# Optimization experiments

Hardware: AMD Instinct MI355X
Metric: run time of the kernel (lower is better)

## Reference

```python
import jax, jax.numpy as jnp
import numpy as np
from jax.ops import segment_sum

N_NODES = 100000


def _gcn_layer(x, W, b, src, dst, n_nodes):
    # DGL GraphConv with norm='both': out = D_in^{-1/2} A D_out^{-1/2} x W + b
    # degrees clamped to min 1 (DGL behavior, handles zero-degree nodes)
    ones_e = jnp.ones(src.shape[0], dtype=x.dtype)
    deg_out = jnp.clip(segment_sum(ones_e, src, num_segments=n_nodes), 1.0)
    deg_in = jnp.clip(segment_sum(ones_e, dst, num_segments=n_nodes), 1.0)
    h = x * jax.lax.rsqrt(deg_out)[:, None]            # [N, F] source norm
    agg = segment_sum(h[src], dst, num_segments=n_nodes)  # [N, F] sum over in-edges
    agg = agg * jax.lax.rsqrt(deg_in)[:, None]          # dest norm
    return agg @ W + b


def setup_inputs() -> dict:
    key = jax.random.key(0)
    k1, k2, k3, k4, k5 = jax.random.split(key, 5)
    E = 1600000
    x = jax.random.normal(k1, (N_NODES, 128), dtype=jnp.float32)
    edge_src = jax.random.randint(k2, (E,), 0, N_NODES, dtype=jnp.int32)
    edge_dst = jax.random.randint(k3, (E,), 0, N_NODES, dtype=jnp.int32)
    W1 = jax.random.normal(k4, (128, 64), dtype=jnp.float32) * (1.0 / np.sqrt(128))
    b1 = jnp.zeros((64,), dtype=jnp.float32)
    W2 = jax.random.normal(k5, (64, 64), dtype=jnp.float32) * (1.0 / np.sqrt(64))
    b2 = jnp.zeros((64,), dtype=jnp.float32)
    return {"x": x, "edge_src": edge_src, "edge_dst": edge_dst,
            "W1": W1, "b1": b1, "W2": W2, "b2": b2}


def reference(x, edge_src, edge_dst, W1, b1, W2, b2):
    h = _gcn_layer(x, W1, b1, edge_src, edge_dst, N_NODES)
    h = jax.nn.relu(h)
    out = _gcn_layer(h, W2, b2, edge_src, edge_dst, N_NODES)
    return out
```

## Files before the change

kernel.cpp:

```cpp
#include <hip/hip_runtime.h>
#include <hip/hip_fp16.h>


static inline size_t align256(size_t x) { return (x + 255) & ~(size_t)255; }

#define BKT_SHIFT 8
#define BKT_W 256
#define MAX_NBK 400
#define CAP 5120
#define SC_BLOCKS 256
#define SC_THREADS 512

typedef _Float16 f16x8 __attribute__((ext_vector_type(8)));
typedef _Float16 f16x4 __attribute__((ext_vector_type(4)));
typedef float f32x4 __attribute__((ext_vector_type(4)));

__global__ __launch_bounds__(SC_THREADS)
void scatter_atomic_kernel(const int* __restrict__ src, const int* __restrict__ dst,
                           int* __restrict__ gcnt_d, int* __restrict__ gcnt_s,
                           int* __restrict__ ebuf, unsigned char* __restrict__ sbuf,
                           int nbk, int E, int slice_len) {
    __shared__ int hd[MAX_NBK];
    __shared__ int hs[MAX_NBK];
    __shared__ int cur_d[MAX_NBK];
    __shared__ int cur_s[MAX_NBK];
    const int b = blockIdx.x;
    const int t = threadIdx.x;
    for (int i = t; i < nbk; i += SC_THREADS) { hd[i] = 0; hs[i] = 0; }
    __syncthreads();
    const int beg = b * slice_len;
    const int end = min(beg + slice_len, E);
    for (int i = beg + t; i < end; i += SC_THREADS) {
        atomicAdd(&hd[dst[i] >> BKT_SHIFT], 1);
        atomicAdd(&hs[src[i] >> BKT_SHIFT], 1);
    }
    __syncthreads();
    for (int i = t; i < nbk; i += SC_THREADS) {
        int c = hd[i];
        cur_d[i] = i * CAP + (c ? atomicAdd(&gcnt_d[i], c) : 0);
        c = hs[i];
        cur_s[i] = i * CAP + (c ? atomicAdd(&gcnt_s[i], c) : 0);
    }
    __syncthreads();
    for (int i = beg + t; i < end; i += SC_THREADS) {
        int d = dst[i], s = src[i];
        int pd = atomicAdd(&cur_d[d >> BKT_SHIFT], 1);
        ebuf[pd] = ((d & (BKT_W - 1)) << 17) | s;
        int ps = atomicAdd(&cur_s[s >> BKT_SHIFT], 1);
        sbuf[ps] = (unsigned char)(s & (BKT_W - 1));
    }
}

__global__ __launch_bounds__(256)
void bucket_csr_kernel(const int* __restrict__ ebuf,
                       const unsigned char* __restrict__ sbuf,
                       const int* __restrict__ gcnt_d, const int* __restrict__ gcnt_s,
                       int* __restrict__ csr_src,
                       int* __restrict__ cnt_in, int* __restrict__ cnt_out,
                       int* __restrict__ row_ptr,
                       int nbk, int N, int E) {
    __shared__ int cnt[BKT_W];
    __shared__ int rp[BKT_W];
    __shared__ int cur[BKT_W];
    __shared__ int cnts[BKT_W];
    __shared__ int red[256];
    __shared__ int sh_db;
    const int k = blockIdx.x;
    const int lo = k << BKT_SHIFT;
    const int span = min(BKT_W, N - lo);
    const int t = threadIdx.x;

    int s1 = 0;
    for (int i = t; i < k; i += 256) s1 += gcnt_d[i];
    red[t] = s1;
    __syncthreads();
    for (int off = 128; off >= 1; off >>= 1) {
        if (t < off) red[t] += red[t + off];
        __syncthreads();
    }
    if (t == 0) sh_db = red[0];
    __syncthreads();
    const int db = sh_db;
    const int eb = k * CAP, ee = eb + gcnt_d[k];
    const int sb = k * CAP, se = sb + gcnt_s[k];

    cnt[t] = 0; cnts[t] = 0;
    __syncthreads();
    for (int i = eb + t; i < ee; i += 256) atomicAdd(&cnt[ebuf[i] >> 17], 1);
    for (int i = sb + t; i < se; i += 256) atomicAdd(&cnts[sbuf[i]], 1);
    __syncthreads();
    rp[t] = cnt[t];
    __syncthreads();
    for (int off = 1; off < BKT_W; off <<= 1) {
        int v = (t >= off) ? rp[t - off] : 0;
        __syncthreads();
        rp[t] += v;
        __syncthreads();
    }
    if (t < span) {
        row_ptr[lo + t] = db + rp[t] - cnt[t];
        cnt_in[lo + t]  = cnt[t];
        cnt_out[lo + t] = cnts[t];
    }
    __syncthreads();
    cur[t] = db + rp[t] - cnt[t];
    __syncthreads();
    for (int i = eb + t; i < ee; i += 256) {
        int p = ebuf[i];
        int pos = atomicAdd(&cur[p >> 17], 1);
        csr_src[pos] = p & 0x1FFFF;
    }
    if (k == 0 && t == 0) row_ptr[N] = E;
}

template <int K>
__global__ __launch_bounds__(256)
void gemm_scale_kernel(const float* __restrict__ X, const float* __restrict__ W,
                       const int* __restrict__ cnt_out,
                       __half* __restrict__ Y, int N) {
    __shared__ _Float16 Wt[2][64][K + 8];
    const int t = threadIdx.x;
    {
        const int jj = t >> 2;
        const int kb = (t & 3) * (K / 4);
#pragma unroll
        for (int c8 = 0; c8 < K / 4; c8 += 8) {
            float w[8];
#pragma unroll
            for (int m = 0; m < 8; ++m) w[m] = W[(kb + c8 + m) * 64 + jj];
            f16x8 hi8, lo8;
#pragma unroll
            for (int m = 0; m < 8; ++m) {
                const _Float16 h = (_Float16)w[m];
                hi8[m] = h;
                lo8[m] = (_Float16)(w[m] - (float)h);
            }
            *(f16x8*)&Wt[0][jj][kb + c8] = hi8;
            *(f16x8*)&Wt[1][jj][kb + c8] = lo8;
        }
    }
    __syncthreads();

    const int wid  = t >> 6;
    const int lane = t & 63;
    const int col  = lane & 15;
    const int kg   = (lane >> 4) * 8;

    const int rowA = blockIdx.x * 64 + wid * 16 + col;
    const size_t xbase = (size_t)min(rowA, N - 1) * K;

    f32x4 acc0 = {}, acc1 = {}, acc2 = {}, acc3 = {};

#pragma unroll
    for (int ks = 0; ks < K; ks += 32) {
        float4 xa = *(const float4*)&X[xbase + ks + kg];
        float4 xb = *(const float4*)&X[xbase + ks + kg + 4];
        const float xs[8] = {xa.x, xa.y, xa.z, xa.w, xb.x, xb.y, xb.z, xb.w};
        f16x8 ahi, alo;
#pragma unroll
        for (int j = 0; j < 8; ++j) {
            const _Float16 h = (_Float16)xs[j];
            ahi[j] = h;
            alo[j] = (_Float16)(xs[j] - (float)h);
        }
#pragma unroll
        for (int tile = 0; tile < 4; ++tile) {
            const f16x8 bhi = *(const f16x8*)&Wt[0][col + 16 * tile][ks + kg];
            const f16x8 blo = *(const f16x8*)&Wt[1][col + 16 * tile][ks + kg];
            f32x4* acc = (tile == 0) ? &acc0 : (tile == 1) ? &acc1
                       : (tile == 2) ? &acc2 : &acc3;
            *acc = __builtin_amdgcn_mfma_f32_16x16x32_f16(ahi, bhi, *acc, 0, 0, 0);
            *acc = __builtin_amdgcn_mfma_f32_16x16x32_f16(alo, bhi, *acc, 0, 0, 0);
            *acc = __builtin_amdgcn_mfma_f32_16x16x32_f16(ahi, blo, *acc, 0, 0, 0);
        }
    }

    const int rbase = blockIdx.x * 64 + wid * 16 + (lane >> 4) * 4;
#pragma unroll
    for (int r = 0; r < 4; ++r) {
        const int rr = rbase + r;
        if (rr < N) {
            const float sc = rsqrtf((float)max(cnt_out[rr], 1));
            __half* yp = &Y[(size_t)rr * 64 + col];
            yp[0]  = __float2half_rn(acc0[r] * sc);
            yp[16] = __float2half_rn(acc1[r] * sc);
            yp[32] = __float2half_rn(acc2[r] * sc);
            yp[48] = __float2half_rn(acc3[r] * sc);
        }
    }
}

__global__ __launch_bounds__(256)
void agg_gemm_kernel(const __half* __restrict__ Y,
                     const int* __restrict__ row_ptr,
                     const int* __restrict__ csr_src,
                     const int* __restrict__ cnt_in,
                     const int* __restrict__ cnt_out,
                     const float* __restrict__ b1,
                     const float* __restrict__ W2,
                     __half* __restrict__ Y2, int N) {
    __shared__ _Float16 Hh[16][72];
    __shared__ _Float16 Hl[16][72];
    const int t = threadIdx.x;
    const int wid  = t >> 6;
    const int lane = t & 63;
    const int col  = lane & 15;
    const int kg   = (lane >> 4) * 8;

    const int nl = t >> 4;
    const int fq = t & 15;
    const int n  = blockIdx.x * 16 + nl;
    const int nc = min(n, N - 1);

    const int start = row_ptr[nc];
    const int end   = row_ptr[nc + 1];
    const int last  = end - 1;

    float4 acc = {0.f, 0.f, 0.f, 0.f};
    for (int e = start; e < end; e += 12) {
        int idx[12];
#pragma unroll
        for (int j = 0; j < 12; ++j) idx[j] = csr_src[min(e + j, last)];
        uint2 v[12];
#pragma unroll
        for (int j = 0; j < 12; ++j)
            v[j] = *((const uint2*)(Y + ((size_t)idx[j] << 6)) + fq);
#pragma unroll
        for (int j = 0; j < 12; ++j) {
            if (e + j < end) {
                float2 a = __half22float2(*(const __half2*)&v[j].x);
                float2 b = __half22float2(*(const __half2*)&v[j].y);
                acc.x += a.x; acc.y += a.y; acc.z += b.x; acc.w += b.y;
            }
        }
    }

    float wb[16];
#pragma unroll
    for (int m = 0; m < 8; ++m) {
        wb[m]     = W2[(kg + m) * 64 + 16 * wid + col];
        wb[m + 8] = W2[(32 + kg + m) * 64 + 16 * wid + col];
    }

    {
        const float sc = rsqrtf((float)max(cnt_in[nc], 1));
        const float4 bb = *(const float4*)&b1[4 * fq];
        float hv[4];
        hv[0] = fmaxf(acc.x * sc + bb.x, 0.f);
        hv[1] = fmaxf(acc.y * sc + bb.y, 0.f);
        hv[2] = fmaxf(acc.z * sc + bb.z, 0.f);
        hv[3] = fmaxf(acc.w * sc + bb.w, 0.f);
        f16x4 hh, hl;
#pragma unroll
        for (int q = 0; q < 4; ++q) {
            const _Float16 hi = (_Float16)hv[q];
            hh[q] = hi;
            hl[q] = (_Float16)(hv[q] - (float)hi);
        }
        *(f16x4*)&Hh[nl][4 * fq] = hh;
        *(f16x4*)&Hl[nl][4 * fq] = hl;
    }
    __syncthreads();

    f16x8 bhi0, blo0, bhi1, blo1;
#pragma unroll
    for (int m = 0; m < 8; ++m) {
        _Float16 h = (_Float16)wb[m];
        bhi0[m] = h;
        blo0[m] = (_Float16)(wb[m] - (float)h);
        h = (_Float16)wb[m + 8];
        bhi1[m] = h;
        blo1[m] = (_Float16)(wb[m + 8] - (float)h);
    }

    const f16x8 ahi0 = *(const f16x8*)&Hh[col][kg];
    const f16x8 alo0 = *(const f16x8*)&Hl[col][kg];
    const f16x8 ahi1 = *(const f16x8*)&Hh[col][32 + kg];
    const f16x8 alo1 = *(const f16x8*)&Hl[col][32 + kg];

    f32x4 acc2 = {};
    acc2 = __builtin_amdgcn_mfma_f32_16x16x32_f16(ahi0, bhi0, acc2, 0, 0, 0);
    acc2 = __builtin_amdgcn_mfma_f32_16x16x32_f16(alo0, bhi0, acc2, 0, 0, 0);
    acc2 = __builtin_amdgcn_mfma_f32_16x16x32_f16(ahi0, blo0, acc2, 0, 0, 0);
    acc2 = __builtin_amdgcn_mfma_f32_16x16x32_f16(ahi1, bhi1, acc2, 0, 0, 0);
    acc2 = __builtin_amdgcn_mfma_f32_16x16x32_f16(alo1, bhi1, acc2, 0, 0, 0);
    acc2 = __builtin_amdgcn_mfma_f32_16x16x32_f16(ahi1, blo1, acc2, 0, 0, 0);

    const int rloc = (lane >> 4) * 4;
#pragma unroll
    for (int r = 0; r < 4; ++r) {
        const int rr = blockIdx.x * 16 + rloc + r;
        if (rr < N) {
            const float s2 = rsqrtf((float)max(cnt_out[rr], 1));
            Y2[(size_t)rr * 64 + 16 * wid + col] = __float2half_rn(acc2[r] * s2);
        }
    }
}

template <bool RELU>
__global__ __launch_bounds__(256)
void aggregate_kernel(const __half* __restrict__ Y,
                      const int* __restrict__ row_ptr,
                      const int* __restrict__ csr_src,
                      const int* __restrict__ cnt_in,
                      const float* __restrict__ bias,
                      float* __restrict__ out, int N) {
    const int n = blockIdx.x * 16 + (threadIdx.x >> 4);
    if (n >= N) return;
    const int fq = threadIdx.x & 15;

    const int start = row_ptr[n];
    const int end   = row_ptr[n + 1];
    const int last  = end - 1;

    float4 acc = {0.f, 0.f, 0.f, 0.f};
    for (int e = start; e < end; e += 12) {
        int idx[12];
#pragma unroll
        for (int j = 0; j < 12; ++j) idx[j] = csr_src[min(e + j, last)];
        uint2 v[12];
#pragma unroll
        for (int j = 0; j < 12; ++j)
            v[j] = *((const uint2*)(Y + ((size_t)idx[j] << 6)) + fq);
#pragma unroll
        for (int j = 0; j < 12; ++j) {
            if (e + j < end) {
                float2 a = __half22float2(*(const __half2*)&v[j].x);
                float2 b = __half22float2(*(const __half2*)&v[j].y);
                acc.x += a.x; acc.y += a.y; acc.z += b.x; acc.w += b.y;
            }
        }
    }

    const float sc = rsqrtf((float)max(cnt_in[n], 1));
    const float4 bb = *(const float4*)&bias[4 * fq];
    float4 o;
    o.x = acc.x * sc + bb.x;
    o.y = acc.y * sc + bb.y;
    o.z = acc.z * sc + bb.z;
    o.w = acc.w * sc + bb.w;
    if (RELU) {
        o.x = fmaxf(o.x, 0.f); o.y = fmaxf(o.y, 0.f);
        o.z = fmaxf(o.z, 0.f); o.w = fmaxf(o.w, 0.f);
    }
    *(float4*)&out[((size_t)n << 6) + 4 * fq] = o;
}

extern "C" void kernel_launch(void* const* d_in, const int* in_sizes, int n_in,
                              void* d_out, int out_size, void* d_ws, size_t ws_size,
                              hipStream_t stream) {
    const float* x   = (const float*)d_in[0];
    const int*   src = (const int*)d_in[1];
    const int*   dst = (const int*)d_in[2];
    const float* W1  = (const float*)d_in[3];
    const float* b1  = (const float*)d_in[4];
    const float* W2  = (const float*)d_in[5];
    const float* b2  = (const float*)d_in[6];
    float* out = (float*)d_out;

    const int N = in_sizes[0] / 128;
    const int E = in_sizes[1];

    const int nbk = (N + BKT_W - 1) >> BKT_SHIFT;

    char* ws = (char*)d_ws;
    size_t off = 0;
    __half* Y       = (__half*)(ws + off); off = align256(off + (size_t)N * 64 * sizeof(__half));
    __half* Y2      = (__half*)(ws + off); off = align256(off + (size_t)N * 64 * sizeof(__half));
    int* csr_src    = (int*)(ws + off);    off = align256(off + (size_t)E * sizeof(int));
    int* ebuf       = (int*)(ws + off);    off = align256(off + (size_t)nbk * CAP * sizeof(int));
    unsigned char* sbuf = (unsigned char*)(ws + off); off = align256(off + (size_t)nbk * CAP);
    int* gcnt       = (int*)(ws + off);    off = align256(off + (size_t)2 * nbk * sizeof(int));
    int* gcnt_d     = gcnt;
    int* gcnt_s     = gcnt + nbk;
    int* cnt_out    = (int*)(ws + off);    off = align256(off + (size_t)N * sizeof(int));
    int* cnt_in     = (int*)(ws + off);    off = align256(off + (size_t)N * sizeof(int));
    int* row_ptr    = (int*)(ws + off);    off = align256(off + (size_t)(N + 1) * sizeof(int));

    const int pslice = (E + SC_BLOCKS - 1) / SC_BLOCKS;

    hipMemsetAsync(gcnt, 0, (size_t)2 * nbk * sizeof(int), stream);
    scatter_atomic_kernel<<<SC_BLOCKS, SC_THREADS, 0, stream>>>(
        src, dst, gcnt_d, gcnt_s, ebuf, sbuf, nbk, E, pslice);
    bucket_csr_kernel<<<nbk, 256, 0, stream>>>(ebuf, sbuf, gcnt_d, gcnt_s, csr_src,
                                               cnt_in, cnt_out, row_ptr, nbk, N, E);

    const int gemm_blocks = (N + 63) / 64;
    const int agg_blocks  = (N + 15) / 16;

    gemm_scale_kernel<128><<<gemm_blocks, 256, 0, stream>>>(x, W1, cnt_out, Y, N);
    agg_gemm_kernel<<<agg_blocks, 256, 0, stream>>>(Y, row_ptr, csr_src,
                                                    cnt_in, cnt_out, b1, W2, Y2, N);
    aggregate_kernel<false><<<agg_blocks, 256, 0, stream>>>(Y2, row_ptr, csr_src,
                                                            cnt_in, b2, out, N);
}
```

Before: 250.0 us.

## Widen gather loads to 16B with 8 lanes per node, 32 nodes per block

```diff
diff --git a/kernel.cpp b/kernel.cpp
--- a/kernel.cpp
+++ b/kernel.cpp
@@ -12,7 +12,6 @@
 #define SC_THREADS 512
 
 typedef _Float16 f16x8 __attribute__((ext_vector_type(8)));
-typedef _Float16 f16x4 __attribute__((ext_vector_type(4)));
 typedef float f32x4 __attribute__((ext_vector_type(4)));
 
 __global__ __launch_bounds__(SC_THREADS)
@@ -51,7 +50,7 @@
     }
 }
 
-__global__ __launch_bounds__(256)
+__global__ __launch_bounds__(512)
 void bucket_csr_kernel(const int* __restrict__ ebuf,
                        const unsigned char* __restrict__ sbuf,
                        const int* __restrict__ gcnt_d, const int* __restrict__ gcnt_s,
@@ -63,7 +62,7 @@
     __shared__ int rp[BKT_W];
     __shared__ int cur[BKT_W];
     __shared__ int cnts[BKT_W];
-    __shared__ int red[256];
+    __shared__ int red[512];
     __shared__ int sh_db;
     const int k = blockIdx.x;
     const int lo = k << BKT_SHIFT;
@@ -71,10 +70,10 @@
     const int t = threadIdx.x;
 
     int s1 = 0;
-    for (int i = t; i < k; i += 256) s1 += gcnt_d[i];
+    for (int i = t; i < k; i += 512) s1 += gcnt_d[i];
     red[t] = s1;
     __syncthreads();
-    for (int off = 128; off >= 1; off >>= 1) {
+    for (int off = 256; off >= 1; off >>= 1) {
         if (t < off) red[t] += red[t + off];
         __syncthreads();
     }
@@ -84,17 +83,17 @@
     const int eb = k * CAP, ee = eb + gcnt_d[k];
     const int sb = k * CAP, se = sb + gcnt_s[k];
 
-    cnt[t] = 0; cnts[t] = 0;
-    __syncthreads();
-    for (int i = eb + t; i < ee; i += 256) atomicAdd(&cnt[ebuf[i] >> 17], 1);
-    for (int i = sb + t; i < se; i += 256) atomicAdd(&cnts[sbuf[i]], 1);
-    __syncthreads();
-    rp[t] = cnt[t];
+    if (t < BKT_W) { cnt[t] = 0; cnts[t] = 0; }
+    __syncthreads();
+    for (int i = eb + t; i < ee; i += 512) atomicAdd(&cnt[ebuf[i] >> 17], 1);
+    for (int i = sb + t; i < se; i += 512) atomicAdd(&cnts[sbuf[i]], 1);
+    __syncthreads();
+    if (t < BKT_W) rp[t] = cnt[t];
     __syncthreads();
     for (int off = 1; off < BKT_W; off <<= 1) {
-        int v = (t >= off) ? rp[t - off] : 0;
+        int v = (t < BKT_W && t >= off) ? rp[t - off] : 0;
         __syncthreads();
-        rp[t] += v;
+        if (t < BKT_W) rp[t] += v;
         __syncthreads();
     }
     if (t < span) {
@@ -103,9 +102,9 @@
         cnt_out[lo + t] = cnts[t];
     }
     __syncthreads();
-    cur[t] = db + rp[t] - cnt[t];
-    __syncthreads();
-    for (int i = eb + t; i < ee; i += 256) {
+    if (t < BKT_W) cur[t] = db + rp[t] - cnt[t];
+    __syncthreads();
+    for (int i = eb + t; i < ee; i += 512) {
         int p = ebuf[i];
         int pos = atomicAdd(&cur[p >> 17], 1);
         csr_src[pos] = p & 0x1FFFF;
@@ -199,38 +198,41 @@
                      const float* __restrict__ b1,
                      const float* __restrict__ W2,
                      __half* __restrict__ Y2, int N) {
-    __shared__ _Float16 Hh[16][72];
-    __shared__ _Float16 Hl[16][72];
+    __shared__ _Float16 Hh[32][72];
+    __shared__ _Float16 Hl[32][72];
     const int t = threadIdx.x;
     const int wid  = t >> 6;
     const int lane = t & 63;
     const int col  = lane & 15;
     const int kg   = (lane >> 4) * 8;
 
-    const int nl = t >> 4;
-    const int fq = t & 15;
-    const int n  = blockIdx.x * 16 + nl;
+    const int nl = t >> 3;
+    const int f8 = t & 7;
+    const int n  = blockIdx.x * 32 + nl;
     const int nc = min(n, N - 1);
 
     const int start = row_ptr[nc];
     const int end   = row_ptr[nc + 1];
     const int last  = end - 1;
 
-    float4 acc = {0.f, 0.f, 0.f, 0.f};
-    for (int e = start; e < end; e += 12) {
-        int idx[12];
-#pragma unroll
-        for (int j = 0; j < 12; ++j) idx[j] = csr_src[min(e + j, last)];
-        uint2 v[12];
-#pragma unroll
-        for (int j = 0; j < 12; ++j)
-            v[j] = *((const uint2*)(Y + ((size_t)idx[j] << 6)) + fq);
-#pragma unroll
-        for (int j = 0; j < 12; ++j) {
+    float4 acc0 = {0.f, 0.f, 0.f, 0.f}, acc1 = {0.f, 0.f, 0.f, 0.f};
+    for (int e = start; e < end; e += 8) {
+        int idx[8];
+#pragma unroll
+        for (int j = 0; j < 8; ++j) idx[j] = csr_src[min(e + j, last)];
+        uint4 v[8];
+#pragma unroll
+        for (int j = 0; j < 8; ++j)
+            v[j] = *((const uint4*)(Y + ((size_t)idx[j] << 6)) + f8);
+#pragma unroll
+        for (int j = 0; j < 8; ++j) {
             if (e + j < end) {
                 float2 a = __half22float2(*(const __half2*)&v[j].x);
                 float2 b = __half22float2(*(const __half2*)&v[j].y);
-                acc.x += a.x; acc.y += a.y; acc.z += b.x; acc.w += b.y;
+                float2 c = __half22float2(*(const __half2*)&v[j].z);
+                float2 d = __half22float2(*(const __half2*)&v[j].w);
+                acc0.x += a.x; acc0.y += a.y; acc0.z += b.x; acc0.w += b.y;
+                acc1.x += c.x; acc1.y += c.y; acc1.z += d.x; acc1.w += d.y;
             }
         }
     }
@@ -244,21 +246,26 @@
 
     {
         const float sc = rsqrtf((float)max(cnt_in[nc], 1));
-        const float4 bb = *(const float4*)&b1[4 * fq];
-        float hv[4];
-        hv[0] = fmaxf(acc.x * sc + bb.x, 0.f);
-        hv[1] = fmaxf(acc.y * sc + bb.y, 0.f);
-        hv[2] = fmaxf(acc.z * sc + bb.z, 0.f);
-        hv[3] = fmaxf(acc.w * sc + bb.w, 0.f);
-        f16x4 hh, hl;
-#pragma unroll
-        for (int q = 0; q < 4; ++q) {
+        const float4 bb0 = *(const float4*)&b1[8 * f8];
+        const float4 bb1 = *(const float4*)&b1[8 * f8 + 4];
+        float hv[8];
+        hv[0] = fmaxf(acc0.x * sc + bb0.x, 0.f);
+        hv[1] = fmaxf(acc0.y * sc + bb0.y, 0.f);
+        hv[2] = fmaxf(acc0.z * sc + bb0.z, 0.f);
+        hv[3] = fmaxf(acc0.w * sc + bb0.w, 0.f);
+        hv[4] = fmaxf(acc1.x * sc + bb1.x, 0.f);
+        hv[5] = fmaxf(acc1.y * sc + bb1.y, 0.f);
+        hv[6] = fmaxf(acc1.z * sc + bb1.z, 0.f);
+        hv[7] = fmaxf(acc1.w * sc + bb1.w, 0.f);
+        f16x8 hh, hl;
+#pragma unroll
+        for (int q = 0; q < 8; ++q) {
             const _Float16 hi = (_Float16)hv[q];
             hh[q] = hi;
             hl[q] = (_Float16)(hv[q] - (float)hi);
         }
-        *(f16x4*)&Hh[nl][4 * fq] = hh;
-        *(f16x4*)&Hl[nl][4 * fq] = hl;
+        *(f16x8*)&Hh[nl][8 * f8] = hh;
+        *(f16x8*)&Hl[nl][8 * f8] = hl;
     }
     __syncthreads();
 
@@ -273,26 +280,29 @@
         blo1[m] = (_Float16)(wb[m + 8] - (float)h);
     }
 
-    const f16x8 ahi0 = *(const f16x8*)&Hh[col][kg];
-    const f16x8 alo0 = *(const f16x8*)&Hl[col][kg];
-    const f16x8 ahi1 = *(const f16x8*)&Hh[col][32 + kg];
-    const f16x8 alo1 = *(const f16x8*)&Hl[col][32 + kg];
-
-    f32x4 acc2 = {};
-    acc2 = __builtin_amdgcn_mfma_f32_16x16x32_f16(ahi0, bhi0, acc2, 0, 0, 0);
-    acc2 = __builtin_amdgcn_mfma_f32_16x16x32_f16(alo0, bhi0, acc2, 0, 0, 0);
-    acc2 = __builtin_amdgcn_mfma_f32_16x16x32_f16(ahi0, blo0, acc2, 0, 0, 0);
-    acc2 = __builtin_amdgcn_mfma_f32_16x16x32_f16(ahi1, bhi1, acc2, 0, 0, 0);
-    acc2 = __builtin_amdgcn_mfma_f32_16x16x32_f16(alo1, bhi1, acc2, 0, 0, 0);
-    acc2 = __builtin_amdgcn_mfma_f32_16x16x32_f16(ahi1, blo1, acc2, 0, 0, 0);
-
     const int rloc = (lane >> 4) * 4;
 #pragma unroll
-    for (int r = 0; r < 4; ++r) {
-        const int rr = blockIdx.x * 16 + rloc + r;
-        if (rr < N) {
-            const float s2 = rsqrtf((float)max(cnt_out[rr], 1));
-            Y2[(size_t)rr * 64 + 16 * wid + col] = __float2half_rn(acc2[r] * s2);
+    for (int g = 0; g < 2; ++g) {
+        const f16x8 ahi0 = *(const f16x8*)&Hh[g * 16 + col][kg];
+        const f16x8 alo0 = *(const f16x8*)&Hl[g * 16 + col][kg];
+        const f16x8 ahi1 = *(const f16x8*)&Hh[g * 16 + col][32 + kg];
+        const f16x8 alo1 = *(const f16x8*)&Hl[g * 16 + col][32 + kg];
+
+        f32x4 acc2 = {};
+        acc2 = __builtin_amdgcn_mfma_f32_16x16x32_f16(ahi0, bhi0, acc2, 0, 0, 0);
+        acc2 = __builtin_amdgcn_mfma_f32_16x16x32_f16(alo0, bhi0, acc2, 0, 0, 0);
+        acc2 = __builtin_amdgcn_mfma_f32_16x16x32_f16(ahi0, blo0, acc2, 0, 0, 0);
+        acc2 = __builtin_amdgcn_mfma_f32_16x16x32_f16(ahi1, bhi1, acc2, 0, 0, 0);
+        acc2 = __builtin_amdgcn_mfma_f32_16x16x32_f16(alo1, bhi1, acc2, 0, 0, 0);
+        acc2 = __builtin_amdgcn_mfma_f32_16x16x32_f16(ahi1, blo1, acc2, 0, 0, 0);
+
+#pragma unroll
+        for (int r = 0; r < 4; ++r) {
+            const int rr = blockIdx.x * 32 + g * 16 + rloc + r;
+            if (rr < N) {
+                const float s2 = rsqrtf((float)max(cnt_out[rr], 1));
+                Y2[(size_t)rr * 64 + 16 * wid + col] = __float2half_rn(acc2[r] * s2);
+            }
         }
     }
 }
@@ -305,45 +315,57 @@
                       const int* __restrict__ cnt_in,
                       const float* __restrict__ bias,
                       float* __restrict__ out, int N) {
-    const int n = blockIdx.x * 16 + (threadIdx.x >> 4);
+    const int n = blockIdx.x * 32 + (threadIdx.x >> 3);
     if (n >= N) return;
-    const int fq = threadIdx.x & 15;
+    const int f8 = threadIdx.x & 7;
 
     const int start = row_ptr[n];
     const int end   = row_ptr[n + 1];
     const int last  = end - 1;
 
-    float4 acc = {0.f, 0.f, 0.f, 0.f};
-    for (int e = start; e < end; e += 12) {
-        int idx[12];
-#pragma unroll
-        for (int j = 0; j < 12; ++j) idx[j] = csr_src[min(e + j, last)];
-        uint2 v[12];
-#pragma unroll
-        for (int j = 0; j < 12; ++j)
-            v[j] = *((const uint2*)(Y + ((size_t)idx[j] << 6)) + fq);
-#pragma unroll
-        for (int j = 0; j < 12; ++j) {
+    float4 acc0 = {0.f, 0.f, 0.f, 0.f}, acc1 = {0.f, 0.f, 0.f, 0.f};
+    for (int e = start; e < end; e += 8) {
+        int idx[8];
+#pragma unroll
+        for (int j = 0; j < 8; ++j) idx[j] = csr_src[min(e + j, last)];
+        uint4 v[8];
+#pragma unroll
+        for (int j = 0; j < 8; ++j)
+            v[j] = *((const uint4*)(Y + ((size_t)idx[j] << 6)) + f8);
+#pragma unroll
+        for (int j = 0; j < 8; ++j) {
             if (e + j < end) {
                 float2 a = __half22float2(*(const __half2*)&v[j].x);
                 float2 b = __half22float2(*(const __half2*)&v[j].y);
-                acc.x += a.x; acc.y += a.y; acc.z += b.x; acc.w += b.y;
+                float2 c = __half22float2(*(const __half2*)&v[j].z);
+                float2 d = __half22float2(*(const __half2*)&v[j].w);
+                acc0.x += a.x; acc0.y += a.y; acc0.z += b.x; acc0.w += b.y;
+                acc1.x += c.x; acc1.y += c.y; acc1.z += d.x; acc1.w += d.y;
             }
         }
     }
 
     const float sc = rsqrtf((float)max(cnt_in[n], 1));
-    const float4 bb = *(const float4*)&bias[4 * fq];
-    float4 o;
-    o.x = acc.x * sc + bb.x;
-    o.y = acc.y * sc + bb.y;
-    o.z = acc.z * sc + bb.z;
-    o.w = acc.w * sc + bb.w;
+    const float4 bb0 = *(const float4*)&bias[8 * f8];
+    const float4 bb1 = *(const float4*)&bias[8 * f8 + 4];
+    float4 o0, o1;
+    o0.x = acc0.x * sc + bb0.x;
+    o0.y = acc0.y * sc + bb0.y;
+    o0.z = acc0.z * sc + bb0.z;
+    o0.w = acc0.w * sc + bb0.w;
+    o1.x = acc1.x * sc + bb1.x;
+    o1.y = acc1.y * sc + bb1.y;
+    o1.z = acc1.z * sc + bb1.z;
+    o1.w = acc1.w * sc + bb1.w;
     if (RELU) {
-        o.x = fmaxf(o.x, 0.f); o.y = fmaxf(o.y, 0.f);
-        o.z = fmaxf(o.z, 0.f); o.w = fmaxf(o.w, 0.f);
-    }
-    *(float4*)&out[((size_t)n << 6) + 4 * fq] = o;
+        o0.x = fmaxf(o0.x, 0.f); o0.y = fmaxf(o0.y, 0.f);
+        o0.z = fmaxf(o0.z, 0.f); o0.w = fmaxf(o0.w, 0.f);
+        o1.x = fmaxf(o1.x, 0.f); o1.y = fmaxf(o1.y, 0.f);
+        o1.z = fmaxf(o1.z, 0.f); o1.w = fmaxf(o1.w, 0.f);
+    }
+    float4* op = (float4*)&out[((size_t)n << 6) + 8 * f8];
+    op[0] = o0;
+    op[1] = o1;
 }
 
 extern "C" void kernel_launch(void* const* d_in, const int* in_sizes, int n_in,
@@ -382,11 +404,11 @@
     hipMemsetAsync(gcnt, 0, (size_t)2 * nbk * sizeof(int), stream);
     scatter_atomic_kernel<<<SC_BLOCKS, SC_THREADS, 0, stream>>>(
         src, dst, gcnt_d, gcnt_s, ebuf, sbuf, nbk, E, pslice);
-    bucket_csr_kernel<<<nbk, 256, 0, stream>>>(ebuf, sbuf, gcnt_d, gcnt_s, csr_src,
+    bucket_csr_kernel<<<nbk, 512, 0, stream>>>(ebuf, sbuf, gcnt_d, gcnt_s, csr_src,
                                                cnt_in, cnt_out, row_ptr, nbk, N, E);
 
     const int gemm_blocks = (N + 63) / 64;
-    const int agg_blocks  = (N + 15) / 16;
+    const int agg_blocks  = (N + 31) / 32;
 
     gemm_scale_kernel<128><<<gemm_blocks, 256, 0, stream>>>(x, W1, cnt_out, Y, N);
     agg_gemm_kernel<<<agg_blocks, 256, 0, stream>>>(Y, row_ptr, csr_src,
```

After: 240.6 us. 3.8% less time.
